# Optimization experiments

Hardware: AMD Instinct MI355X
Metric: run time of the kernel (lower is better)

Reference implementation:

```python
import jax, jax.numpy as jnp
import numpy as np

N = 131072          # total sampled proposals (flattened over batch)
D = 1024            # num_extractor_out
C = 21              # num_classes (VOC: 20 + background)


def setup_inputs() -> dict:
    key = jax.random.key(0)
    k1, k2, k3 = jax.random.split(key, 3)
    features = jax.random.normal(k1, (N, D), dtype=jnp.float32)
    # Linear weights stored as [in, out] so y = x @ W + b
    W_cls = jax.random.normal(k2, (D, C), dtype=jnp.float32) * (1.0 / np.sqrt(D))
    b_cls = jnp.zeros((C,), dtype=jnp.float32)
    W_tf = jax.random.normal(k3, (D, C * 4), dtype=jnp.float32) * (1.0 / np.sqrt(D))
    b_tf = jnp.zeros((C * 4,), dtype=jnp.float32)
    return {"features": features, "W_cls": W_cls, "b_cls": b_cls, "W_tf": W_tf, "b_tf": b_tf}


def reference(features, W_cls, b_cls, W_tf, b_tf):
    # ROI.forward with identity extractor / no pre/post transforms.
    proposal_classes = features @ W_cls + b_cls                    # [N, C]
    proposal_transformers = features @ W_tf + b_tf                 # [N, C*4]
    proposal_transformers = proposal_transformers.reshape(features.shape[0], C, 4)
    return proposal_classes, proposal_transformers
```

## Files before the change

kernel.cpp:

```cpp
#include <hip/hip_runtime.h>
#include <hip/hip_bf16.h>

#define NROWS 131072
#define DK    1024
#define CCLS  21
#define CTF   84
#define NCOL  105
#define NKT   (DK/32)
#define NCT   7

#define BM    128
#define LDA   40

typedef __attribute__((ext_vector_type(4))) float f32x4;
typedef __attribute__((ext_vector_type(8))) short bf16x8;
typedef __attribute__((ext_vector_type(4))) short bf16x4;

__device__ __forceinline__ unsigned short f2bf(float x) {
    union { float f; unsigned u; } v; v.f = x;
    unsigned r = v.u + 0x7fffu + ((v.u >> 16) & 1u);
    return (unsigned short)(r >> 16);
}

__global__ void pack_B_kernel(const float* __restrict__ Wc,
                              const float* __restrict__ Wt,
                              unsigned short* __restrict__ Bp) {
    const int frag = blockIdx.x;
    const int kt = frag / NCT, ct = frag % NCT;
    const int lane = threadIdx.x;
    const int col = ct * 16 + (lane & 15);
    const int k0  = kt * 32 + ((lane >> 4) << 3);
    bf16x8 o;
#pragma unroll
    for (int j = 0; j < 8; ++j) {
        const int k = k0 + j;
        float v = 0.0f;
        if (col < CCLS)      v = Wc[k * CCLS + col];
        else if (col < NCOL) v = Wt[k * CTF + (col - CCLS)];
        o[j] = (short)f2bf(v);
    }
    *reinterpret_cast<bf16x8*>(Bp + ((size_t)frag * 64 + lane) * 8) = o;
}

__global__ __launch_bounds__(256)
void roi_gemm_kernel(const float* __restrict__ F,
                     const unsigned short* __restrict__ Bp,
                     const float* __restrict__ bcls,
                     const float* __restrict__ btf,
                     float* __restrict__ out) {
    __shared__ unsigned short Alds[2][BM * LDA];

    const int t    = threadIdx.x;
    const int wave = t >> 6;
    const int lane = t & 63;
    const long row0 = (long)blockIdx.x * BM;

    const int srow = t >> 3;
    const int scol = (t & 7) * 4;

    const int fr = lane & 15;
    const int fk = (lane >> 4) * 8;

    f32x4 acc[2][NCT];
#pragma unroll
    for (int a = 0; a < 2; ++a)
#pragma unroll
        for (int b = 0; b < NCT; ++b)
            acc[a][b] = (f32x4){0.f, 0.f, 0.f, 0.f};

    const float* Fb = F + (size_t)row0 * DK;

#pragma unroll
    for (int i = 0; i < 4; ++i) {
        const f32x4 v = *reinterpret_cast<const f32x4*>(Fb + (size_t)(srow + 32 * i) * DK + scol);
        bf16x4 w;
#pragma unroll
        for (int j = 0; j < 4; ++j) w[j] = (short)f2bf(v[j]);
        *reinterpret_cast<bf16x4*>(&Alds[0][(srow + 32 * i) * LDA + scol]) = w;
    }
    __syncthreads();

    for (int kt = 0; kt < NKT; ++kt) {
        const int cur = kt & 1;

        f32x4 nx[4];
        if (kt + 1 < NKT) {
#pragma unroll
            for (int i = 0; i < 4; ++i)
                nx[i] = *reinterpret_cast<const f32x4*>(
                    Fb + (size_t)(srow + 32 * i) * DK + (size_t)(kt + 1) * 32 + scol);
        }

        bf16x8 bfrag[NCT];
        const unsigned short* bb = Bp + ((size_t)kt * NCT * 64 + lane) * 8;
#pragma unroll
        for (int ct = 0; ct < NCT; ++ct)
            bfrag[ct] = *reinterpret_cast<const bf16x8*>(bb + (size_t)ct * 64 * 8);

        bf16x8 afrag[2];
#pragma unroll
        for (int rt = 0; rt < 2; ++rt) {
            const int r = wave * 32 + rt * 16 + fr;
            afrag[rt] = *reinterpret_cast<const bf16x8*>(&Alds[cur][r * LDA + fk]);
        }

#pragma unroll
        for (int rt = 0; rt < 2; ++rt)
#pragma unroll
            for (int ct = 0; ct < NCT; ++ct)
                acc[rt][ct] = __builtin_amdgcn_mfma_f32_16x16x32_bf16(
                    afrag[rt], bfrag[ct], acc[rt][ct], 0, 0, 0);

        if (kt + 1 < NKT) {
#pragma unroll
            for (int i = 0; i < 4; ++i) {
                bf16x4 w;
#pragma unroll
                for (int j = 0; j < 4; ++j) w[j] = (short)f2bf(nx[i][j]);
                *reinterpret_cast<bf16x4*>(&Alds[cur ^ 1][(srow + 32 * i) * LDA + scol]) = w;
            }
        }
        __syncthreads();
    }

    float* out_tf = out + (size_t)NROWS * CCLS;
#pragma unroll
    for (int rt = 0; rt < 2; ++rt) {
        const long rbase = row0 + wave * 32 + rt * 16 + ((lane >> 4) << 2);
#pragma unroll
        for (int ct = 0; ct < NCT; ++ct) {
            const int col = ct * 16 + (lane & 15);
            if (col >= NCOL) continue;
            const float bias = (col < CCLS) ? bcls[col] : btf[col - CCLS];
#pragma unroll
            for (int j = 0; j < 4; ++j) {
                const long row = rbase + j;
                const float v = acc[rt][ct][j] + bias;
                if (col < CCLS) out[row * CCLS + col] = v;
                else            out_tf[row * CTF + (col - CCLS)] = v;
            }
        }
    }
}

extern "C" void kernel_launch(void* const* d_in, const int* in_sizes, int n_in,
                              void* d_out, int out_size, void* d_ws, size_t ws_size,
                              hipStream_t stream) {
    const float* F  = (const float*)d_in[0];
    const float* Wc = (const float*)d_in[1];
    const float* bc = (const float*)d_in[2];
    const float* Wt = (const float*)d_in[3];
    const float* bt = (const float*)d_in[4];
    unsigned short* Bp = (unsigned short*)d_ws;

    pack_B_kernel<<<NKT * NCT, 64, 0, stream>>>(Wc, Wt, Bp);
    roi_gemm_kernel<<<NROWS / BM, 256, 0, stream>>>(F, Bp, bc, bt, (float*)d_out);
}
```

Measured before the change: 166.5 us.

## Load A fragments straight from global into registers, dropping LDS staging

```diff
diff --git a/kernel.cpp b/kernel.cpp
--- a/kernel.cpp
+++ b/kernel.cpp
@@ -8,18 +8,29 @@
 #define NCOL  105
 #define NKT   (DK/32)
 #define NCT   7
-
 #define BM    128
-#define LDA   40
 
 typedef __attribute__((ext_vector_type(4))) float f32x4;
 typedef __attribute__((ext_vector_type(8))) short bf16x8;
-typedef __attribute__((ext_vector_type(4))) short bf16x4;
 
-__device__ __forceinline__ unsigned short f2bf(float x) {
+__device__ __forceinline__ unsigned short f2bf_rne(float x) {
     union { float f; unsigned u; } v; v.f = x;
     unsigned r = v.u + 0x7fffu + ((v.u >> 16) & 1u);
     return (unsigned short)(r >> 16);
+}
+
+__device__ __forceinline__ unsigned pack2(float lo, float hi) {
+    union { float f; unsigned u; } a, b; a.f = lo; b.f = hi;
+    return ((a.u + 0x8000u) >> 16) | ((b.u + 0x8000u) & 0xffff0000u);
+}
+
+__device__ __forceinline__ bf16x8 cvt8(const f32x4 lo, const f32x4 hi) {
+    union { unsigned u[4]; bf16x8 v; } r;
+    r.u[0] = pack2(lo[0], lo[1]);
+    r.u[1] = pack2(lo[2], lo[3]);
+    r.u[2] = pack2(hi[0], hi[1]);
+    r.u[3] = pack2(hi[2], hi[3]);
+    return r.v;
 }
 
 __global__ void pack_B_kernel(const float* __restrict__ Wc,
@@ -37,29 +48,26 @@
         float v = 0.0f;
         if (col < CCLS)      v = Wc[k * CCLS + col];
         else if (col < NCOL) v = Wt[k * CTF + (col - CCLS)];
-        o[j] = (short)f2bf(v);
+        o[j] = (short)f2bf_rne(v);
     }
     *reinterpret_cast<bf16x8*>(Bp + ((size_t)frag * 64 + lane) * 8) = o;
 }
 
-__global__ __launch_bounds__(256)
+__global__ __launch_bounds__(256, 4)
 void roi_gemm_kernel(const float* __restrict__ F,
                      const unsigned short* __restrict__ Bp,
                      const float* __restrict__ bcls,
                      const float* __restrict__ btf,
                      float* __restrict__ out) {
-    __shared__ unsigned short Alds[2][BM * LDA];
-
     const int t    = threadIdx.x;
     const int wave = t >> 6;
     const int lane = t & 63;
-    const long row0 = (long)blockIdx.x * BM;
+    const int fr   = lane & 15;
+    const int fk   = (lane >> 4) * 8;
 
-    const int srow = t >> 3;
-    const int scol = (t & 7) * 4;
-
-    const int fr = lane & 15;
-    const int fk = (lane >> 4) * 8;
+    const long rw = (long)blockIdx.x * BM + wave * 32;
+    const float* pa0 = F + (size_t)(rw + fr) * DK + fk;
+    const float* pa1 = pa0 + (size_t)16 * DK;
 
     f32x4 acc[2][NCT];
 #pragma unroll
@@ -68,68 +76,39 @@
         for (int b = 0; b < NCT; ++b)
             acc[a][b] = (f32x4){0.f, 0.f, 0.f, 0.f};
 
-    const float* Fb = F + (size_t)row0 * DK;
+    const unsigned short* bb = Bp + (size_t)lane * 8;
+
+    for (int kt = 0; kt < NKT; ++kt) {
+        const f32x4 a0lo = *reinterpret_cast<const f32x4*>(pa0 + kt * 32);
+        const f32x4 a0hi = *reinterpret_cast<const f32x4*>(pa0 + kt * 32 + 4);
+        const f32x4 a1lo = *reinterpret_cast<const f32x4*>(pa1 + kt * 32);
+        const f32x4 a1hi = *reinterpret_cast<const f32x4*>(pa1 + kt * 32 + 4);
+
+        bf16x8 bfrag[NCT];
+#pragma unroll
+        for (int ct = 0; ct < NCT; ++ct)
+            bfrag[ct] = *reinterpret_cast<const bf16x8*>(
+                bb + ((size_t)kt * NCT + ct) * 64 * 8);
+
+        const bf16x8 af0 = cvt8(a0lo, a0hi);
+        const bf16x8 af1 = cvt8(a1lo, a1hi);
 
 #pragma unroll
-    for (int i = 0; i < 4; ++i) {
-        const f32x4 v = *reinterpret_cast<const f32x4*>(Fb + (size_t)(srow + 32 * i) * DK + scol);
-        bf16x4 w;
-#pragma unroll
-        for (int j = 0; j < 4; ++j) w[j] = (short)f2bf(v[j]);
-        *reinterpret_cast<bf16x4*>(&Alds[0][(srow + 32 * i) * LDA + scol]) = w;
-    }
-    __syncthreads();
-
-    for (int kt = 0; kt < NKT; ++kt) {
-        const int cur = kt & 1;
-
-        f32x4 nx[4];
-        if (kt + 1 < NKT) {
-#pragma unroll
-            for (int i = 0; i < 4; ++i)
-                nx[i] = *reinterpret_cast<const f32x4*>(
-                    Fb + (size_t)(srow + 32 * i) * DK + (size_t)(kt + 1) * 32 + scol);
+        for (int ct = 0; ct < NCT; ++ct) {
+            acc[0][ct] = __builtin_amdgcn_mfma_f32_16x16x32_bf16(
+                af0, bfrag[ct], acc[0][ct], 0, 0, 0);
+            acc[1][ct] = __builtin_amdgcn_mfma_f32_16x16x32_bf16(
+                af1, bfrag[ct], acc[1][ct], 0, 0, 0);
         }
-
-        bf16x8 bfrag[NCT];
-        const unsigned short* bb = Bp + ((size_t)kt * NCT * 64 + lane) * 8;
-#pragma unroll
-        for (int ct = 0; ct < NCT; ++ct)
-            bfrag[ct] = *reinterpret_cast<const bf16x8*>(bb + (size_t)ct * 64 * 8);
-
-        bf16x8 afrag[2];
-#pragma unroll
-        for (int rt = 0; rt < 2; ++rt) {
-            const int r = wave * 32 + rt * 16 + fr;
-            afrag[rt] = *reinterpret_cast<const bf16x8*>(&Alds[cur][r * LDA + fk]);
-        }
-
-#pragma unroll
-        for (int rt = 0; rt < 2; ++rt)
-#pragma unroll
-            for (int ct = 0; ct < NCT; ++ct)
-                acc[rt][ct] = __builtin_amdgcn_mfma_f32_16x16x32_bf16(
-                    afrag[rt], bfrag[ct], acc[rt][ct], 0, 0, 0);
-
-        if (kt + 1 < NKT) {
-#pragma unroll
-            for (int i = 0; i < 4; ++i) {
-                bf16x4 w;
-#pragma unroll
-                for (int j = 0; j < 4; ++j) w[j] = (short)f2bf(nx[i][j]);
-                *reinterpret_cast<bf16x4*>(&Alds[cur ^ 1][(srow + 32 * i) * LDA + scol]) = w;
-            }
-        }
-        __syncthreads();
     }
 
     float* out_tf = out + (size_t)NROWS * CCLS;
 #pragma unroll
     for (int rt = 0; rt < 2; ++rt) {
-        const long rbase = row0 + wave * 32 + rt * 16 + ((lane >> 4) << 2);
+        const long rbase = rw + rt * 16 + ((lane >> 4) << 2);
 #pragma unroll
         for (int ct = 0; ct < NCT; ++ct) {
-            const int col = ct * 16 + (lane & 15);
+            const int col = ct * 16 + fr;
             if (col >= NCOL) continue;
             const float bias = (col < CCLS) ? bcls[col] : btf[col - CCLS];
 #pragma unroll
```

Result: slower. 172.1 us (+3.4%).
